# Kernel optimization log

Measured on AMD Instinct MI355X. Metric: run time of the kernel, lower is better.

Reference implementation:

```python
import jax, jax.numpy as jnp
import numpy as np

D_MODEL = 512
N_HEADS = 8
D_FF = 2048

def _linear_params(key, d_in, d_out):
    kw, kb = jax.random.split(key)
    bound = 1.0 / np.sqrt(d_in)
    W = jax.random.uniform(kw, (d_in, d_out), minval=-bound, maxval=bound, dtype=jnp.float32)
    b = jax.random.uniform(kb, (d_out,), minval=-bound, maxval=bound, dtype=jnp.float32)
    return W, b

def setup_inputs() -> dict:
    key = jax.random.key(0)
    ks = jax.random.split(key, 7)
    x = jax.random.normal(ks[0], (4, 2048, D_MODEL), dtype=jnp.float32)
    Wq, bq = _linear_params(ks[1], D_MODEL, D_MODEL)
    Wk, bk = _linear_params(ks[2], D_MODEL, D_MODEL)
    Wv, bv = _linear_params(ks[3], D_MODEL, D_MODEL)
    W1, b1 = _linear_params(ks[4], D_MODEL, D_FF)
    W2, b2 = _linear_params(ks[5], D_FF, D_MODEL)
    g1 = jnp.ones((D_MODEL,), jnp.float32); be1 = jnp.zeros((D_MODEL,), jnp.float32)
    g2 = jnp.ones((D_MODEL,), jnp.float32); be2 = jnp.zeros((D_MODEL,), jnp.float32)
    return {"x": x, "Wq": Wq, "bq": bq, "Wk": Wk, "bk": bk, "Wv": Wv, "bv": bv,
            "W1": W1, "b1": b1, "W2": W2, "b2": b2,
            "g1": g1, "be1": be1, "g2": g2, "be2": be2}

def _layernorm(x, g, b, eps=1e-5):
    mu = jnp.mean(x, axis=-1, keepdims=True)
    var = jnp.mean(jnp.square(x - mu), axis=-1, keepdims=True)
    return (x - mu) * jax.lax.rsqrt(var + eps) * g + b

def reference(x, Wq, bq, Wk, bk, Wv, bv, W1, b1, W2, b2, g1, be1, g2, be2):
    B, S, D = x.shape
    H = N_HEADS
    Dh = D // H
    residual = x
    xn = _layernorm(x, g1, be1)
    # [B,S,D] -> [B,H,S,Dh]
    q = (xn @ Wq + bq).reshape(B, S, H, Dh).transpose(0, 2, 1, 3)
    k = (xn @ Wk + bk).reshape(B, S, H, Dh).transpose(0, 2, 1, 3)
    v = (xn @ Wv + bv).reshape(B, S, H, Dh).transpose(0, 2, 1, 3)
    # sigmoid pointwise attention, scaled by sqrt(d_model) (not head dim)
    scores = jnp.einsum('bhsd,bhtd->bhst', q, k) / jnp.sqrt(jnp.float32(D))
    attn = jax.nn.sigmoid(scores)
    out = jnp.einsum('bhst,bhtd->bhsd', attn, v)
    out = out.transpose(0, 2, 1, 3).reshape(B, S, D)
    x = residual + out  # dropout=0 (eval)
    residual = x
    xn = _layernorm(x, g2, be2)
    ffn = jax.nn.relu(xn @ W1 + b1) @ W2 + b2
    return residual + ffn
```

## Files before the change

### kernel.cpp

```cpp
#include <hip/hip_runtime.h>
#include <hip/hip_bf16.h>
#include <math.h>

#define D_MODEL 512
#define N_HEADS 8
#define D_HEAD 64
#define D_FF 2048
#define SEQ 2048
#define BATCH 4
#define NTOK (BATCH * SEQ)
#define QSCALE 0.04419417382415922f

typedef unsigned short ushort_t;
typedef __attribute__((ext_vector_type(8))) short short8;
typedef __attribute__((ext_vector_type(4))) float float4v;

static __device__ __forceinline__ ushort_t f2bf(float f) {
    union { float f; unsigned int i; } c; c.f = f;
    unsigned int i = c.i;
    unsigned int r = (i + 0x7FFFu + ((i >> 16) & 1u)) >> 16;
    return (ushort_t)r;
}

static __device__ __forceinline__ unsigned int pack2bf(float a, float b) {
    union { __hip_bfloat162 h; unsigned int u; } c;
    c.h = __float22bfloat162_rn(make_float2(a, b));
    return c.u;
}

static __device__ __forceinline__ float sigmoid_f(float x) {
    return __builtin_amdgcn_rcpf(1.0f + __expf(-x));
}

__global__ __launch_bounds__(256) void k_transpose_w(const float* __restrict__ W,
                                                     ushort_t* __restrict__ Wt,
                                                     int K, int N) {
    int id = blockIdx.x * 256 + threadIdx.x;
    if (id >= K * N) return;
    int k = id / N, n = id - k * N;
    Wt[(size_t)n * K + k] = f2bf(W[id]);
}

__global__ __launch_bounds__(256) void k_layernorm(const float* __restrict__ X,
                                                   const float* __restrict__ g,
                                                   const float* __restrict__ be,
                                                   ushort_t* __restrict__ Out) {
    int row  = blockIdx.x * 4 + (threadIdx.x >> 6);
    int lane = threadIdx.x & 63;
    const float* x = X + (size_t)row * D_MODEL + lane * 8;
    float4 v0 = ((const float4*)x)[0];
    float4 v1 = ((const float4*)x)[1];
    float vals[8] = {v0.x, v0.y, v0.z, v0.w, v1.x, v1.y, v1.z, v1.w};
    float s = 0.f, sq = 0.f;
#pragma unroll
    for (int j = 0; j < 8; j++) { s += vals[j]; sq += vals[j] * vals[j]; }
#pragma unroll
    for (int off = 32; off; off >>= 1) { s += __shfl_xor(s, off); sq += __shfl_xor(sq, off); }
    float mu  = s * (1.0f / D_MODEL);
    float var = sq * (1.0f / D_MODEL) - mu * mu;
    float inv = rsqrtf(var + 1e-5f);
    const float* gp  = g  + lane * 8;
    const float* bp  = be + lane * 8;
    float4 g0 = ((const float4*)gp)[0], g1v = ((const float4*)gp)[1];
    float4 b0 = ((const float4*)bp)[0], b1v = ((const float4*)bp)[1];
    float gs[8] = {g0.x, g0.y, g0.z, g0.w, g1v.x, g1v.y, g1v.z, g1v.w};
    float bs[8] = {b0.x, b0.y, b0.z, b0.w, b1v.x, b1v.y, b1v.z, b1v.w};
    ushort_t o[8];
#pragma unroll
    for (int j = 0; j < 8; j++) o[j] = f2bf((vals[j] - mu) * inv * gs[j] + bs[j]);
    ushort_t* op = Out + (size_t)row * D_MODEL + lane * 8;
    *(uint4*)op = *(uint4*)o;
}

__device__ __forceinline__ void gemm_core(const ushort_t* __restrict__ A,
                                          const ushort_t* __restrict__ Bt,
                                          int K, int m0, int n0,
                                          ushort_t (*As)[128][40], ushort_t (*Bs)[128][40],
                                          float4v acc[4][4]) {
    int t = threadIdx.x, w = t >> 6, l = t & 63, q = l >> 4, lm = l & 15;
    int mb = (w & 1) * 64, nb = (w >> 1) * 64;
    int srow = t >> 1, scol = (t & 1) * 16;
    const ushort_t* ag0 = A  + (size_t)(m0 + srow) * K + scol;
    const ushort_t* bg0 = Bt + (size_t)(n0 + srow) * K + scol;

    uint4 ar0 = *(const uint4*)(ag0),     ar1 = *(const uint4*)(ag0 + 8);
    uint4 br0 = *(const uint4*)(bg0),     br1 = *(const uint4*)(bg0 + 8);
    *(uint4*)&As[0][srow][scol] = ar0; *(uint4*)&As[0][srow][scol + 8] = ar1;
    *(uint4*)&Bs[0][srow][scol] = br0; *(uint4*)&Bs[0][srow][scol + 8] = br1;
    int T = K >> 5;
    ar0 = *(const uint4*)(ag0 + 32); ar1 = *(const uint4*)(ag0 + 40);
    br0 = *(const uint4*)(bg0 + 32); br1 = *(const uint4*)(bg0 + 40);
    __syncthreads();

    for (int kt = 0; kt < T; kt++) {
        int cur = kt & 1;
        short8 a[4], b[4];
#pragma unroll
        for (int i = 0; i < 4; i++) a[i] = *(const short8*)&As[cur][mb + 16 * i + lm][q * 8];
#pragma unroll
        for (int j = 0; j < 4; j++) b[j] = *(const short8*)&Bs[cur][nb + 16 * j + lm][q * 8];
#pragma unroll
        for (int i = 0; i < 4; i++)
#pragma unroll
            for (int j = 0; j < 4; j++)
                acc[i][j] = __builtin_amdgcn_mfma_f32_16x16x32_bf16(a[i], b[j], acc[i][j], 0, 0, 0);
        if (kt + 1 < T) {
            int nxt = 1 - cur;
            *(uint4*)&As[nxt][srow][scol] = ar0; *(uint4*)&As[nxt][srow][scol + 8] = ar1;
            *(uint4*)&Bs[nxt][srow][scol] = br0; *(uint4*)&Bs[nxt][srow][scol + 8] = br1;
            if (kt + 2 < T) {
                const ushort_t* ag = ag0 + (kt + 2) * 32;
                const ushort_t* bg = bg0 + (kt + 2) * 32;
                ar0 = *(const uint4*)(ag); ar1 = *(const uint4*)(ag + 8);
                br0 = *(const uint4*)(bg); br1 = *(const uint4*)(bg + 8);
            }
        }
        __syncthreads();
    }
}

__global__ __launch_bounds__(256) void k_gemm_qkv(const ushort_t* __restrict__ A,
                                                  const ushort_t* __restrict__ Bt,
                                                  const float* __restrict__ bq,
                                                  const float* __restrict__ bk,
                                                  const float* __restrict__ bv,
                                                  ushort_t* __restrict__ qb,
                                                  ushort_t* __restrict__ kb,
                                                  ushort_t* __restrict__ vt) {
    __shared__ ushort_t As[2][128][40];
    __shared__ ushort_t Bs[2][128][40];
    int m0 = blockIdx.x * 128, n0 = blockIdx.y * 128;
    float4v acc[4][4];
#pragma unroll
    for (int i = 0; i < 4; i++)
#pragma unroll
        for (int j = 0; j < 4; j++) acc[i][j] = (float4v){0.f, 0.f, 0.f, 0.f};
    gemm_core(A, Bt, D_MODEL, m0, n0, As, Bs, acc);

    int t = threadIdx.x, w = t >> 6, l = t & 63, q = l >> 4, lm = l & 15;
    int mb = (w & 1) * 64, nb = (w >> 1) * 64;
    int mat = n0 >> 9, c0 = n0 & 511;
    const float* bias = (mat == 0) ? bq : ((mat == 1) ? bk : bv);
#pragma unroll
    for (int j = 0; j < 4; j++) {
        int cl = c0 + nb + 16 * j + lm;
        int hh = cl >> 6, dh = cl & 63;
        float bvv = bias[cl];
#pragma unroll
        for (int i = 0; i < 4; i++) {
            int mr0 = m0 + mb + 16 * i + q * 4;
            int bb = mr0 >> 11, ss0 = mr0 & (SEQ - 1);
            if (mat == 2) {
                union { ushort_t s[4]; uint2 v; } pk;
#pragma unroll
                for (int r = 0; r < 4; r++) pk.s[r] = f2bf(acc[i][j][r] + bvv);
                *(uint2*)&vt[((size_t)(bb * N_HEADS + hh) * D_HEAD + dh) * SEQ + ss0] = pk.v;
            } else {
                ushort_t* dst = (mat == 0) ? qb : kb;
                float sc = (mat == 0) ? QSCALE : 1.0f;
#pragma unroll
                for (int r = 0; r < 4; r++)
                    dst[((size_t)(bb * N_HEADS + hh) * SEQ + ss0 + r) * D_HEAD + dh] =
                        f2bf((acc[i][j][r] + bvv) * sc);
            }
        }
    }
}

__global__ __launch_bounds__(256) void k_gemm_ffn1(const ushort_t* __restrict__ A,
                                                   const ushort_t* __restrict__ Bt,
                                                   const float* __restrict__ b1,
                                                   ushort_t* __restrict__ hb) {
    __shared__ ushort_t As[2][128][40];
    __shared__ ushort_t Bs[2][128][40];
    int m0 = blockIdx.x * 128, n0 = blockIdx.y * 128;
    float4v acc[4][4];
#pragma unroll
    for (int i = 0; i < 4; i++)
#pragma unroll
        for (int j = 0; j < 4; j++) acc[i][j] = (float4v){0.f, 0.f, 0.f, 0.f};
    gemm_core(A, Bt, D_MODEL, m0, n0, As, Bs, acc);

    int t = threadIdx.x, w = t >> 6, l = t & 63, q = l >> 4, lm = l & 15;
    int mb = (w & 1) * 64, nb = (w >> 1) * 64;
#pragma unroll
    for (int j = 0; j < 4; j++) {
        int cl = n0 + nb + 16 * j + lm;
        float bvv = b1[cl];
#pragma unroll
        for (int i = 0; i < 4; i++) {
            int mr0 = m0 + mb + 16 * i + q * 4;
#pragma unroll
            for (int r = 0; r < 4; r++)
                hb[(size_t)(mr0 + r) * D_FF + cl] = f2bf(fmaxf(acc[i][j][r] + bvv, 0.f));
        }
    }
}

__global__ __launch_bounds__(256) void k_gemm_ffn2(const ushort_t* __restrict__ A,
                                                   const ushort_t* __restrict__ Bt,
                                                   const float* __restrict__ b2,
                                                   const float* __restrict__ res,
                                                   float* __restrict__ out) {
    __shared__ ushort_t As[2][128][40];
    __shared__ ushort_t Bs[2][128][40];
    int m0 = blockIdx.x * 128, n0 = blockIdx.y * 128;
    float4v acc[4][4];
#pragma unroll
    for (int i = 0; i < 4; i++)
#pragma unroll
        for (int j = 0; j < 4; j++) acc[i][j] = (float4v){0.f, 0.f, 0.f, 0.f};
    gemm_core(A, Bt, D_FF, m0, n0, As, Bs, acc);

    int t = threadIdx.x, w = t >> 6, l = t & 63, q = l >> 4, lm = l & 15;
    int mb = (w & 1) * 64, nb = (w >> 1) * 64;
#pragma unroll
    for (int j = 0; j < 4; j++) {
        int cl = n0 + nb + 16 * j + lm;
        float bvv = b2[cl];
#pragma unroll
        for (int i = 0; i < 4; i++) {
            int mr0 = m0 + mb + 16 * i + q * 4;
#pragma unroll
            for (int r = 0; r < 4; r++) {
                size_t idx = (size_t)(mr0 + r) * D_MODEL + cl;
                out[idx] = acc[i][j][r] + bvv + res[idx];
            }
        }
    }
}

__global__ __launch_bounds__(256) void k_attention(const ushort_t* __restrict__ Q,
                                                   const ushort_t* __restrict__ Kb,
                                                   const ushort_t* __restrict__ Vt,
                                                   const float* __restrict__ X,
                                                   float* __restrict__ Y) {
    __shared__ ushort_t Ks[2][64][72];
    __shared__ ushort_t Vs[2][64][72];
    __shared__ ushort_t Ps[128][72];
    int bh = blockIdx.y;
    int b = bh >> 3, h = bh & 7;
    size_t base = (size_t)bh * SEQ * D_HEAD;
    int s0 = blockIdx.x * 128;
    int t = threadIdx.x, w = t >> 6, l = t & 63, q = l >> 4, lm = l & 15;
    int srow = t >> 2, sc = (t & 3) * 16;

    short8 qf[2][2];
#pragma unroll
    for (int nt = 0; nt < 2; nt++)
#pragma unroll
        for (int kc = 0; kc < 2; kc++) {
            const ushort_t* qg = Q + base + (size_t)(s0 + 32 * w + 16 * nt + lm) * D_HEAD + kc * 32 + q * 8;
            uint4 u = *(const uint4*)qg;
            qf[nt][kc] = *(const short8*)&u;
        }

    float4v o[2][4];
#pragma unroll
    for (int nt = 0; nt < 2; nt++)
#pragma unroll
        for (int dj = 0; dj < 4; dj++) o[nt][dj] = (float4v){0.f, 0.f, 0.f, 0.f};

    uint4 kr0, kr1, vr0, vr1;
    const ushort_t* kg0 = Kb + base + (size_t)srow * D_HEAD + sc;
    const ushort_t* vg0 = Vt + base + (size_t)srow * SEQ + sc;

    kr0 = *(const uint4*)(kg0); kr1 = *(const uint4*)(kg0 + 8);
    vr0 = *(const uint4*)(vg0); vr1 = *(const uint4*)(vg0 + 8);
    *(uint4*)&Ks[0][srow][sc] = kr0; *(uint4*)&Ks[0][srow][sc + 8] = kr1;
    *(uint4*)&Vs[0][srow][sc] = vr0; *(uint4*)&Vs[0][srow][sc + 8] = vr1;
    kr0 = *(const uint4*)(kg0 + 64 * D_HEAD); kr1 = *(const uint4*)(kg0 + 64 * D_HEAD + 8);
    vr0 = *(const uint4*)(vg0 + 64);          vr1 = *(const uint4*)(vg0 + 64 + 8);
    __syncthreads();

    for (int tt = 0; tt < SEQ / 64; tt++) {
        int cur = tt & 1;
        float4v st[4][2];
#pragma unroll
        for (int mt = 0; mt < 4; mt++)
#pragma unroll
            for (int nt = 0; nt < 2; nt++) st[mt][nt] = (float4v){0.f, 0.f, 0.f, 0.f};
#pragma unroll
        for (int kc = 0; kc < 2; kc++) {
            short8 a[4];
#pragma unroll
            for (int mt = 0; mt < 4; mt++) a[mt] = *(const short8*)&Ks[cur][16 * mt + lm][kc * 32 + q * 8];
#pragma unroll
            for (int mt = 0; mt < 4; mt++)
#pragma unroll
                for (int nt = 0; nt < 2; nt++)
                    st[mt][nt] = __builtin_amdgcn_mfma_f32_16x16x32_bf16(a[mt], qf[nt][kc], st[mt][nt], 0, 0, 0);
        }
#pragma unroll
        for (int mt = 0; mt < 4; mt++)
#pragma unroll
            for (int nt = 0; nt < 2; nt++) {
                float4v s4 = st[mt][nt];
                uint2 pk;
                pk.x = pack2bf(sigmoid_f(s4[0]), sigmoid_f(s4[1]));
                pk.y = pack2bf(sigmoid_f(s4[2]), sigmoid_f(s4[3]));
                *(uint2*)&Ps[32 * w + 16 * nt + lm][16 * mt + 4 * q] = pk;
            }
#pragma unroll
        for (int kc = 0; kc < 2; kc++) {
            short8 ap[2], bv[4];
#pragma unroll
            for (int nt = 0; nt < 2; nt++) ap[nt] = *(const short8*)&Ps[32 * w + 16 * nt + lm][kc * 32 + q * 8];
#pragma unroll
            for (int dj = 0; dj < 4; dj++) bv[dj] = *(const short8*)&Vs[cur][16 * dj + lm][kc * 32 + q * 8];
#pragma unroll
            for (int nt = 0; nt < 2; nt++)
#pragma unroll
                for (int dj = 0; dj < 4; dj++)
                    o[nt][dj] = __builtin_amdgcn_mfma_f32_16x16x32_bf16(ap[nt], bv[dj], o[nt][dj], 0, 0, 0);
        }
        if (tt + 1 < SEQ / 64) {
            int nxt = 1 - cur;
            *(uint4*)&Ks[nxt][srow][sc] = kr0; *(uint4*)&Ks[nxt][srow][sc + 8] = kr1;
            *(uint4*)&Vs[nxt][srow][sc] = vr0; *(uint4*)&Vs[nxt][srow][sc + 8] = vr1;
            if (tt + 2 < SEQ / 64) {
                const ushort_t* kg = kg0 + (size_t)(tt + 2) * 64 * D_HEAD;
                const ushort_t* vg = vg0 + (tt + 2) * 64;
                kr0 = *(const uint4*)(kg); kr1 = *(const uint4*)(kg + 8);
                vr0 = *(const uint4*)(vg); vr1 = *(const uint4*)(vg + 8);
            }
        }
        __syncthreads();
    }

#pragma unroll
    for (int nt = 0; nt < 2; nt++)
#pragma unroll
        for (int dj = 0; dj < 4; dj++) {
            int d = 16 * dj + lm;
#pragma unroll
            for (int r = 0; r < 4; r++) {
                int s = s0 + 32 * w + 16 * nt + q * 4 + r;
                size_t idx = ((size_t)(b * SEQ + s)) * D_MODEL + h * D_HEAD + d;
                Y[idx] = X[idx] + o[nt][dj][r];
            }
        }
}

extern "C" void kernel_launch(void* const* d_in, const int* in_sizes, int n_in,
                              void* d_out, int out_size, void* d_ws, size_t ws_size,
                              hipStream_t stream) {
    const float* x   = (const float*)d_in[0];
    const float* Wq  = (const float*)d_in[1];
    const float* bq  = (const float*)d_in[2];
    const float* Wk  = (const float*)d_in[3];
    const float* bk  = (const float*)d_in[4];
    const float* Wv  = (const float*)d_in[5];
    const float* bv  = (const float*)d_in[6];
    const float* W1  = (const float*)d_in[7];
    const float* b1  = (const float*)d_in[8];
    const float* W2  = (const float*)d_in[9];
    const float* b2  = (const float*)d_in[10];
    const float* g1  = (const float*)d_in[11];
    const float* be1 = (const float*)d_in[12];
    const float* g2  = (const float*)d_in[13];
    const float* be2 = (const float*)d_in[14];
    float* out = (float*)d_out;

    char* p = (char*)d_ws;
    ushort_t* xn    = (ushort_t*)p; p += (size_t)NTOK * D_MODEL * 2;
    ushort_t* yn    = (ushort_t*)p; p += (size_t)NTOK * D_MODEL * 2;
    float*    y     = (float*)p;    p += (size_t)NTOK * D_MODEL * 4;
    ushort_t* qb    = (ushort_t*)p; p += (size_t)NTOK * D_MODEL * 2;
    ushort_t* kb    = (ushort_t*)p; p += (size_t)NTOK * D_MODEL * 2;
    ushort_t* vt    = (ushort_t*)p; p += (size_t)NTOK * D_MODEL * 2;
    ushort_t* hb    = (ushort_t*)p; p += (size_t)NTOK * D_FF * 2;
    ushort_t* Wqkvt = (ushort_t*)p; p += (size_t)3 * D_MODEL * D_MODEL * 2;
    ushort_t* W1t   = (ushort_t*)p; p += (size_t)D_MODEL * D_FF * 2;
    ushort_t* W2t   = (ushort_t*)p; p += (size_t)D_FF * D_MODEL * 2;

    k_transpose_w<<<(D_MODEL * D_MODEL + 255) / 256, 256, 0, stream>>>(Wq, Wqkvt, D_MODEL, D_MODEL);
    k_transpose_w<<<(D_MODEL * D_MODEL + 255) / 256, 256, 0, stream>>>(Wk, Wqkvt + (size_t)D_MODEL * D_MODEL, D_MODEL, D_MODEL);
    k_transpose_w<<<(D_MODEL * D_MODEL + 255) / 256, 256, 0, stream>>>(Wv, Wqkvt + (size_t)2 * D_MODEL * D_MODEL, D_MODEL, D_MODEL);
    k_transpose_w<<<(D_MODEL * D_FF + 255) / 256, 256, 0, stream>>>(W1, W1t, D_MODEL, D_FF);
    k_transpose_w<<<(D_FF * D_MODEL + 255) / 256, 256, 0, stream>>>(W2, W2t, D_FF, D_MODEL);

    k_layernorm<<<NTOK / 4, 256, 0, stream>>>(x, g1, be1, xn);

    dim3 gq(NTOK / 128, (3 * D_MODEL) / 128);
    k_gemm_qkv<<<gq, 256, 0, stream>>>(xn, Wqkvt, bq, bk, bv, qb, kb, vt);

    dim3 ga(SEQ / 128, BATCH * N_HEADS);
    k_attention<<<ga, 256, 0, stream>>>(qb, kb, vt, x, y);

    k_layernorm<<<NTOK / 4, 256, 0, stream>>>(y, g2, be2, yn);

    dim3 g1d(NTOK / 128, D_FF / 128);
    k_gemm_ffn1<<<g1d, 256, 0, stream>>>(yn, W1t, b1, hb);
    dim3 g2d(NTOK / 128, D_MODEL / 128);
    k_gemm_ffn2<<<g2d, 256, 0, stream>>>(hb, W2t, b2, y, out);
}
```

Measured before the change: 275.0 us.

## Use direct global-to-LDS loads in GEMMs, fuse weight prep, exp2 sigmoid

```diff
diff --git a/kernel.cpp b/kernel.cpp
--- a/kernel.cpp
+++ b/kernel.cpp
@@ -10,6 +10,7 @@
 #define BATCH 4
 #define NTOK (BATCH * SEQ)
 #define QSCALE 0.04419417382415922f
+#define QSCALE_L2E (-QSCALE * 1.44269504089f)
 
 typedef unsigned short ushort_t;
 typedef __attribute__((ext_vector_type(8))) short short8;
@@ -28,17 +29,37 @@
     return c.u;
 }
 
-static __device__ __forceinline__ float sigmoid_f(float x) {
-    return __builtin_amdgcn_rcpf(1.0f + __expf(-x));
-}
-
-__global__ __launch_bounds__(256) void k_transpose_w(const float* __restrict__ W,
-                                                     ushort_t* __restrict__ Wt,
-                                                     int K, int N) {
+static __device__ __forceinline__ float sig2(float x) {
+    return __builtin_amdgcn_rcpf(1.0f + __builtin_amdgcn_exp2f(x));
+}
+
+__global__ __launch_bounds__(256) void k_prep_weights(const float* __restrict__ Wq,
+                                                      const float* __restrict__ Wk,
+                                                      const float* __restrict__ Wv,
+                                                      const float* __restrict__ W1,
+                                                      const float* __restrict__ W2,
+                                                      ushort_t* __restrict__ Wqkvt,
+                                                      ushort_t* __restrict__ W1t,
+                                                      ushort_t* __restrict__ W2t) {
     int id = blockIdx.x * 256 + threadIdx.x;
-    if (id >= K * N) return;
-    int k = id / N, n = id - k * N;
-    Wt[(size_t)n * K + k] = f2bf(W[id]);
+    if (id < 3 * 262144) {
+        int m = id >> 18, r = id & 262143;
+        int k = r >> 9, n = r & 511;
+        const float* src = (m == 0) ? Wq : ((m == 1) ? Wk : Wv);
+        Wqkvt[((size_t)m * 512 + n) * 512 + k] = f2bf(src[r]);
+        return;
+    }
+    int id2 = id - 3 * 262144;
+    if (id2 < 1048576) {
+        int k = id2 >> 11, n = id2 & 2047;
+        W1t[(size_t)n * 512 + k] = f2bf(W1[id2]);
+        return;
+    }
+    int id3 = id2 - 1048576;
+    if (id3 < 1048576) {
+        int k = id3 >> 9, n = id3 & 511;
+        W2t[(size_t)n * 2048 + k] = f2bf(W2[id3]);
+    }
 }
 
 __global__ __launch_bounds__(256) void k_layernorm(const float* __restrict__ X,
@@ -72,49 +93,54 @@
     *(uint4*)op = *(uint4*)o;
 }
 
-__device__ __forceinline__ void gemm_core(const ushort_t* __restrict__ A,
-                                          const ushort_t* __restrict__ Bt,
-                                          int K, int m0, int n0,
-                                          ushort_t (*As)[128][40], ushort_t (*Bs)[128][40],
-                                          float4v acc[4][4]) {
+
+static __device__ __forceinline__ void stage_tile(const ushort_t* __restrict__ G, int K,
+                                                  ushort_t* L, int nchunks, int koff,
+                                                  int w, int l) {
+#pragma unroll
+    for (int n = w; n < nchunks; n += 4) {
+        const ushort_t* g = G + (size_t)(n * 16 + (l >> 2)) * K + koff + (l & 3) * 8;
+        __builtin_amdgcn_global_load_lds((const __attribute__((address_space(1))) void*)g,
+                                         (__attribute__((address_space(3))) void*)(L + n * 512),
+                                         16, 0, 0);
+    }
+}
+
+template <int JW>
+static __device__ __forceinline__ void gemm_core2(const ushort_t* __restrict__ A,
+                                                  const ushort_t* __restrict__ Bt,
+                                                  int K, int m0, int n0,
+                                                  ushort_t* As, ushort_t* Bs,
+                                                  float4v acc[4][JW]) {
+    const int BBUF = JW * 1024;
     int t = threadIdx.x, w = t >> 6, l = t & 63, q = l >> 4, lm = l & 15;
-    int mb = (w & 1) * 64, nb = (w >> 1) * 64;
-    int srow = t >> 1, scol = (t & 1) * 16;
-    const ushort_t* ag0 = A  + (size_t)(m0 + srow) * K + scol;
-    const ushort_t* bg0 = Bt + (size_t)(n0 + srow) * K + scol;
-
-    uint4 ar0 = *(const uint4*)(ag0),     ar1 = *(const uint4*)(ag0 + 8);
-    uint4 br0 = *(const uint4*)(bg0),     br1 = *(const uint4*)(bg0 + 8);
-    *(uint4*)&As[0][srow][scol] = ar0; *(uint4*)&As[0][srow][scol + 8] = ar1;
-    *(uint4*)&Bs[0][srow][scol] = br0; *(uint4*)&Bs[0][srow][scol + 8] = br1;
+    int mb = (w & 1) * 64, nb = (w >> 1) * (JW * 16);
+    const ushort_t* Ab = A + (size_t)m0 * K;
+    const ushort_t* Bb = Bt + (size_t)n0 * K;
     int T = K >> 5;
-    ar0 = *(const uint4*)(ag0 + 32); ar1 = *(const uint4*)(ag0 + 40);
-    br0 = *(const uint4*)(bg0 + 32); br1 = *(const uint4*)(bg0 + 40);
+
+    stage_tile(Ab, K, As, 8, 0, w, l);
+    stage_tile(Bb, K, Bs, 2 * JW, 0, w, l);
     __syncthreads();
 
     for (int kt = 0; kt < T; kt++) {
         int cur = kt & 1;
-        short8 a[4], b[4];
-#pragma unroll
-        for (int i = 0; i < 4; i++) a[i] = *(const short8*)&As[cur][mb + 16 * i + lm][q * 8];
-#pragma unroll
-        for (int j = 0; j < 4; j++) b[j] = *(const short8*)&Bs[cur][nb + 16 * j + lm][q * 8];
+        if (kt + 1 < T) {
+            stage_tile(Ab, K, As + (1 - cur) * 4096, 8, (kt + 1) * 32, w, l);
+            stage_tile(Bb, K, Bs + (1 - cur) * BBUF, 2 * JW, (kt + 1) * 32, w, l);
+        }
+        const ushort_t* asb = As + cur * 4096;
+        const ushort_t* bsb = Bs + cur * BBUF;
+        short8 a[4], b[JW];
+#pragma unroll
+        for (int i = 0; i < 4; i++) a[i] = *(const short8*)&asb[(mb + 16 * i + lm) * 32 + q * 8];
+#pragma unroll
+        for (int j = 0; j < JW; j++) b[j] = *(const short8*)&bsb[(nb + 16 * j + lm) * 32 + q * 8];
 #pragma unroll
         for (int i = 0; i < 4; i++)
 #pragma unroll
-            for (int j = 0; j < 4; j++)
+            for (int j = 0; j < JW; j++)
                 acc[i][j] = __builtin_amdgcn_mfma_f32_16x16x32_bf16(a[i], b[j], acc[i][j], 0, 0, 0);
-        if (kt + 1 < T) {
-            int nxt = 1 - cur;
-            *(uint4*)&As[nxt][srow][scol] = ar0; *(uint4*)&As[nxt][srow][scol + 8] = ar1;
-            *(uint4*)&Bs[nxt][srow][scol] = br0; *(uint4*)&Bs[nxt][srow][scol + 8] = br1;
-            if (kt + 2 < T) {
-                const ushort_t* ag = ag0 + (kt + 2) * 32;
-                const ushort_t* bg = bg0 + (kt + 2) * 32;
-                ar0 = *(const uint4*)(ag); ar1 = *(const uint4*)(ag + 8);
-                br0 = *(const uint4*)(bg); br1 = *(const uint4*)(bg + 8);
-            }
-        }
         __syncthreads();
     }
 }
@@ -127,15 +153,15 @@
                                                   ushort_t* __restrict__ qb,
                                                   ushort_t* __restrict__ kb,
                                                   ushort_t* __restrict__ vt) {
-    __shared__ ushort_t As[2][128][40];
-    __shared__ ushort_t Bs[2][128][40];
+    __shared__ __align__(16) ushort_t As[8192];
+    __shared__ __align__(16) ushort_t Bs[8192];
     int m0 = blockIdx.x * 128, n0 = blockIdx.y * 128;
     float4v acc[4][4];
 #pragma unroll
     for (int i = 0; i < 4; i++)
 #pragma unroll
         for (int j = 0; j < 4; j++) acc[i][j] = (float4v){0.f, 0.f, 0.f, 0.f};
-    gemm_core(A, Bt, D_MODEL, m0, n0, As, Bs, acc);
+    gemm_core2<4>(A, Bt, D_MODEL, m0, n0, As, Bs, acc);
 
     int t = threadIdx.x, w = t >> 6, l = t & 63, q = l >> 4, lm = l & 15;
     int mb = (w & 1) * 64, nb = (w >> 1) * 64;
@@ -157,7 +183,7 @@
                 *(uint2*)&vt[((size_t)(bb * N_HEADS + hh) * D_HEAD + dh) * SEQ + ss0] = pk.v;
             } else {
                 ushort_t* dst = (mat == 0) ? qb : kb;
-                float sc = (mat == 0) ? QSCALE : 1.0f;
+                float sc = (mat == 0) ? QSCALE_L2E : 1.0f;
 #pragma unroll
                 for (int r = 0; r < 4; r++)
                     dst[((size_t)(bb * N_HEADS + hh) * SEQ + ss0 + r) * D_HEAD + dh] =
@@ -171,15 +197,15 @@
                                                    const ushort_t* __restrict__ Bt,
                                                    const float* __restrict__ b1,
                                                    ushort_t* __restrict__ hb) {
-    __shared__ ushort_t As[2][128][40];
-    __shared__ ushort_t Bs[2][128][40];
+    __shared__ __align__(16) ushort_t As[8192];
+    __shared__ __align__(16) ushort_t Bs[8192];
     int m0 = blockIdx.x * 128, n0 = blockIdx.y * 128;
     float4v acc[4][4];
 #pragma unroll
     for (int i = 0; i < 4; i++)
 #pragma unroll
         for (int j = 0; j < 4; j++) acc[i][j] = (float4v){0.f, 0.f, 0.f, 0.f};
-    gemm_core(A, Bt, D_MODEL, m0, n0, As, Bs, acc);
+    gemm_core2<4>(A, Bt, D_MODEL, m0, n0, As, Bs, acc);
 
     int t = threadIdx.x, w = t >> 6, l = t & 63, q = l >> 4, lm = l & 15;
     int mb = (w & 1) * 64, nb = (w >> 1) * 64;
@@ -202,20 +228,20 @@
                                                    const float* __restrict__ b2,
                                                    const float* __restrict__ res,
                                                    float* __restrict__ out) {
-    __shared__ ushort_t As[2][128][40];
-    __shared__ ushort_t Bs[2][128][40];
-    int m0 = blockIdx.x * 128, n0 = blockIdx.y * 128;
-    float4v acc[4][4];
+    __shared__ __align__(16) ushort_t As[8192];
+    __shared__ __align__(16) ushort_t Bs[4096];
+    int m0 = blockIdx.x * 128, n0 = blockIdx.y * 64;
+    float4v acc[4][2];
 #pragma unroll
     for (int i = 0; i < 4; i++)
 #pragma unroll
-        for (int j = 0; j < 4; j++) acc[i][j] = (float4v){0.f, 0.f, 0.f, 0.f};
-    gemm_core(A, Bt, D_FF, m0, n0, As, Bs, acc);
+        for (int j = 0; j < 2; j++) acc[i][j] = (float4v){0.f, 0.f, 0.f, 0.f};
+    gemm_core2<2>(A, Bt, D_FF, m0, n0, As, Bs, acc);
 
     int t = threadIdx.x, w = t >> 6, l = t & 63, q = l >> 4, lm = l & 15;
-    int mb = (w & 1) * 64, nb = (w >> 1) * 64;
-#pragma unroll
-    for (int j = 0; j < 4; j++) {
+    int mb = (w & 1) * 64, nb = (w >> 1) * 32;
+#pragma unroll
+    for (int j = 0; j < 2; j++) {
         int cl = n0 + nb + 16 * j + lm;
         float bvv = b2[cl];
 #pragma unroll
@@ -297,8 +323,8 @@
             for (int nt = 0; nt < 2; nt++) {
                 float4v s4 = st[mt][nt];
                 uint2 pk;
-                pk.x = pack2bf(sigmoid_f(s4[0]), sigmoid_f(s4[1]));
-                pk.y = pack2bf(sigmoid_f(s4[2]), sigmoid_f(s4[3]));
+                pk.x = pack2bf(sig2(s4[0]), sig2(s4[1]));
+                pk.y = pack2bf(sig2(s4[2]), sig2(s4[3]));
                 *(uint2*)&Ps[32 * w + 16 * nt + lm][16 * mt + 4 * q] = pk;
             }
 #pragma unroll
@@ -374,11 +400,8 @@
     ushort_t* W1t   = (ushort_t*)p; p += (size_t)D_MODEL * D_FF * 2;
     ushort_t* W2t   = (ushort_t*)p; p += (size_t)D_FF * D_MODEL * 2;
 
-    k_transpose_w<<<(D_MODEL * D_MODEL + 255) / 256, 256, 0, stream>>>(Wq, Wqkvt, D_MODEL, D_MODEL);
-    k_transpose_w<<<(D_MODEL * D_MODEL + 255) / 256, 256, 0, stream>>>(Wk, Wqkvt + (size_t)D_MODEL * D_MODEL, D_MODEL, D_MODEL);
-    k_transpose_w<<<(D_MODEL * D_MODEL + 255) / 256, 256, 0, stream>>>(Wv, Wqkvt + (size_t)2 * D_MODEL * D_MODEL, D_MODEL, D_MODEL);
-    k_transpose_w<<<(D_MODEL * D_FF + 255) / 256, 256, 0, stream>>>(W1, W1t, D_MODEL, D_FF);
-    k_transpose_w<<<(D_FF * D_MODEL + 255) / 256, 256, 0, stream>>>(W2, W2t, D_FF, D_MODEL);
+    k_prep_weights<<<(3 * 262144 + 2 * 1048576 + 255) / 256, 256, 0, stream>>>(
+        Wq, Wk, Wv, W1, W2, Wqkvt, W1t, W2t);
 
     k_layernorm<<<NTOK / 4, 256, 0, stream>>>(x, g1, be1, xn);
 
@@ -392,6 +415,6 @@
 
     dim3 g1d(NTOK / 128, D_FF / 128);
     k_gemm_ffn1<<<g1d, 256, 0, stream>>>(yn, W1t, b1, hb);
-    dim3 g2d(NTOK / 128, D_MODEL / 128);
+    dim3 g2d(NTOK / 128, D_MODEL / 64);
     k_gemm_ffn2<<<g2d, 256, 0, stream>>>(hb, W2t, b2, y, out);
 }
```

After: 263.0 us. 4.4% less time.
